# Kernel optimization log

Hardware: AMD Instinct MI355X
Metric: run time of the kernel (lower is better)

## Reference

```python
import jax, jax.numpy as jnp
import numpy as np

NHEADS = 8
KSIZE = 15
DILATION = 1


def _local_mask(N, ksize, d):
    # eye(N) + sum_i eye(N, k=+/-(d*i)) for i in 1..ksize//2  -> banded boolean mask
    K = ksize // 2
    m = np.eye(N)
    for i in range(1, K + 1):
        m += np.eye(N, k=d * i) + np.eye(N, k=-d * i)
    return jnp.asarray(m > 0)


def _nl(x, mask, cW, cb, vW, vb, lm):
    """NonLocalBlock: keys from v_lin, queries/values from c_lin split; per-head
    scores mk @ mq^T / sqrt(dh), banded local mask + segment mask, softmax over
    last axis, residual add. drop_prob=0 so dropout is identity."""
    B, L, D = x.shape
    odim = vW.shape[1]
    dh = odim // NHEADS
    neg = jnp.asarray(-1e9, x.dtype)
    mk = (x @ vW + vb).reshape(B, L, NHEADS, dh)
    ct = x @ cW + cb                      # [B,L,2*odim]
    mq = ct[..., :odim].reshape(B, L, NHEADS, dh)
    mv = ct[..., odim:].reshape(B, L, NHEADS, dh)
    s = jnp.einsum('blhd,bmhd->bhlm', mk, mq) / jnp.sqrt(jnp.asarray(dh, x.dtype))
    if lm is not None:
        s = jnp.where(lm[None, None], s, neg)
    s = jnp.where((mask != 0)[:, None, None, :], s, neg)
    w = jax.nn.softmax(s, axis=-1)
    r = jnp.einsum('bhlm,bmhd->blhd', w, mv).reshape(B, L, odim)
    return x + r


def setup_inputs() -> dict:
    key = jax.random.key(0)
    ks = jax.random.split(key, 24)
    B, L, D, N = 16, 512, 512, 3
    NL_LOCAL, NL_GLOBAL, AH = 2, 2, 256
    sc = 0.02
    rn = lambda k, shp: jax.random.normal(k, shp, jnp.float32) * sc
    return {
        'seg_feats': jax.random.normal(ks[0], (B, L, D), jnp.float32),
        'seg_masks': jnp.ones((B, L), jnp.float32),
        'se_feats': jax.random.normal(ks[1], (B, N, D), jnp.float32),
        # HadamardProduct params, one per semantic entity (stacked on axis 0)
        'hp_w1': rn(ks[2], (N, D, D)), 'hp_b1': jnp.zeros((N, D), jnp.float32),
        'hp_w2': rn(ks[3], (N, D, D)), 'hp_b2': jnp.zeros((N, D), jnp.float32),
        'hp_w3': rn(ks[4], (N, D, D)), 'hp_b3': jnp.zeros((N, D), jnp.float32),
        # local masked non-local blocks: [N, n_local_mnl, ...]
        'local_cW': rn(ks[5], (N, NL_LOCAL, D, 2 * D)),
        'local_cb': jnp.zeros((N, NL_LOCAL, 2 * D), jnp.float32),
        'local_vW': rn(ks[6], (N, NL_LOCAL, D, D)),
        'local_vb': jnp.zeros((N, NL_LOCAL, D), jnp.float32),
        # global non-local blocks: [n_global_nl, ...]
        'global_cW': rn(ks[7], (NL_GLOBAL, D, 2 * D)),
        'global_cb': jnp.zeros((NL_GLOBAL, 2 * D), jnp.float32),
        'global_vW': rn(ks[8], (NL_GLOBAL, D, D)),
        'global_vb': jnp.zeros((NL_GLOBAL, D), jnp.float32),
        # AttentivePooling over semantic entities (no bias, no embedding fc)
        'satt_w1': rn(ks[9], (D, AH)),
        'satt_w2': rn(ks[10], (AH, 1)),
    }


def reference(seg_feats, seg_masks, se_feats,
              hp_w1, hp_b1, hp_w2, hp_b2, hp_w3, hp_b3,
              local_cW, local_cb, local_vW, local_vb,
              global_cW, global_cb, global_vW, global_vb,
              satt_w1, satt_w2):
    B, L, D = seg_feats.shape
    N = se_feats.shape[1]
    # 1) segment-level modality fusion (HadamardProduct per semantic entity)
    h1 = jax.nn.relu(jnp.einsum('bld,ndh->bnlh', seg_feats, hp_w1) + hp_b1[None, :, None, :])
    h2 = jax.nn.relu(jnp.einsum('bnd,ndh->bnh', se_feats, hp_w2) + hp_b2[None])
    m = jax.nn.relu(jnp.einsum('bnlh,nhk->bnlk', h1 * h2[:, :, None, :], hp_w3)
                    + hp_b3[None, :, None, :])  # [B,N,L,D]
    # 2) local context modeling: masked non-local blocks with banded mask
    lm = _local_mask(L, KSIZE, DILATION)
    ss = []
    for n in range(N):
        f = m[:, n]
        for s in range(local_cW.shape[1]):
            f = _nl(f, seg_masks, local_cW[n, s], local_cb[n, s],
                    local_vW[n, s], local_vb[n, s], lm)
        ss.append(f)
    ss = jnp.stack(ss, axis=1)  # [B,N,L,D]
    # 3) semantic attentive pooling over entities -> weighted sum of ss_feats
    alpha = jnp.tanh(se_feats @ satt_w1) @ satt_w2       # [B,N,1]
    sattw = jax.nn.softmax(alpha[..., 0], axis=1)        # [B,N]
    a = jnp.einsum('bn,bnld->bld', sattw, ss)            # [B,L,D]
    # 4) global context modeling: plain non-local blocks (no local mask)
    for s in range(global_cW.shape[0]):
        a = _nl(a, seg_masks, global_cW[s], global_cb[s], global_vW[s], global_vb[s], None)
    return a, sattw
```

## Files before the change

### kernel.cpp

```cpp
#include <hip/hip_runtime.h>
#include <hip/hip_bf16.h>

#define BB 16
#define LL 512
#define DD 512
#define NSEG 3
#define NH 8
#define DH 64
#define AH 256

typedef __attribute__((ext_vector_type(4))) float f32x4;
typedef __attribute__((ext_vector_type(8))) short s16x8;

__device__ __forceinline__ unsigned short f2b(float f) {
  union { float f; unsigned u; } c; c.f = f;
  unsigned r = (c.u + 0x7FFF + ((c.u >> 16) & 1)) >> 16;
  return (unsigned short)r;
}

#define PADK 40
__global__ __launch_bounds__(256) void mfma_gemm(
    const float* __restrict__ A, const float* __restrict__ W,
    const float* __restrict__ bias, float* __restrict__ C,
    int Nc, int K, long bsA, long bsC, int act)
{
  __shared__ unsigned short As[64 * PADK];
  __shared__ unsigned short Bs[64 * PADK];
  const int tid = threadIdx.x;
  const int lane = tid & 63, wv = tid >> 6;
  const float* Ab = A + (long)blockIdx.z * bsA + (long)blockIdx.y * 64 * K;
  const float* Wb = W + blockIdx.x * 64;
  float* Cb = C + (long)blockIdx.z * bsC + (long)blockIdx.y * 64 * Nc + blockIdx.x * 64;

  const int arow = tid >> 2, akq = tid & 3;
  const int bkp = tid & 15, bnq = tid >> 4;
  const int fr = lane & 15, fk = (lane >> 4) * 8;

  f32x4 acc[4] = {};
  for (int k0 = 0; k0 < K; k0 += 32) {
    {
      const float* ap = Ab + (long)arow * K + k0 + akq * 8;
      float4 a0 = *(const float4*)ap;
      float4 a1 = *(const float4*)(ap + 4);
      union { unsigned short h[8]; uint4 v; } u;
      u.h[0] = f2b(a0.x); u.h[1] = f2b(a0.y); u.h[2] = f2b(a0.z); u.h[3] = f2b(a0.w);
      u.h[4] = f2b(a1.x); u.h[5] = f2b(a1.y); u.h[6] = f2b(a1.z); u.h[7] = f2b(a1.w);
      *(uint4*)&As[arow * PADK + akq * 8] = u.v;
    }
    {
      const float* wp = Wb + (long)(k0 + 2 * bkp) * Nc + 4 * bnq;
      float4 w0 = *(const float4*)wp;
      float4 w1 = *(const float4*)(wp + Nc);
      unsigned* bsw = (unsigned*)Bs;
      bsw[(4 * bnq + 0) * (PADK / 2) + bkp] = (unsigned)f2b(w0.x) | ((unsigned)f2b(w1.x) << 16);
      bsw[(4 * bnq + 1) * (PADK / 2) + bkp] = (unsigned)f2b(w0.y) | ((unsigned)f2b(w1.y) << 16);
      bsw[(4 * bnq + 2) * (PADK / 2) + bkp] = (unsigned)f2b(w0.z) | ((unsigned)f2b(w1.z) << 16);
      bsw[(4 * bnq + 3) * (PADK / 2) + bkp] = (unsigned)f2b(w0.w) | ((unsigned)f2b(w1.w) << 16);
    }
    __syncthreads();
    s16x8 af = *(const s16x8*)&As[(wv * 16 + fr) * PADK + fk];
#pragma unroll
    for (int nt = 0; nt < 4; ++nt) {
      s16x8 bf = *(const s16x8*)&Bs[(nt * 16 + fr) * PADK + fk];
      acc[nt] = __builtin_amdgcn_mfma_f32_16x16x32_bf16(af, bf, acc[nt], 0, 0, 0);
    }
    __syncthreads();
  }
  const int rowb = wv * 16 + (lane >> 4) * 4;
  const int colb = lane & 15;
#pragma unroll
  for (int nt = 0; nt < 4; ++nt) {
    const float bv = bias[blockIdx.x * 64 + nt * 16 + colb];
#pragma unroll
    for (int j = 0; j < 4; ++j) {
      float v = acc[nt][j] + bv;
      if (act) v = fmaxf(v, 0.f);
      Cb[(long)(rowb + j) * Nc + nt * 16 + colb] = v;
    }
  }
}

__global__ __launch_bounds__(256) void h2_kernel(
    const float* __restrict__ se, const float* __restrict__ w2,
    const float* __restrict__ b2, float* __restrict__ h2)
{
  __shared__ float ses[DD];
  const int bn = blockIdx.x;
  const int n = bn % NSEG;
  const int t = threadIdx.x;
  ses[t] = se[(long)bn * DD + t];
  ses[t + 256] = se[(long)bn * DD + t + 256];
  __syncthreads();
  const float* wn = w2 + (long)n * DD * DD;
  for (int j = t; j < DD; j += 256) {
    float acc = b2[n * DD + j];
    for (int k = 0; k < DD; ++k) acc = fmaf(ses[k], wn[(long)k * DD + j], acc);
    h2[(long)bn * DD + j] = fmaxf(acc, 0.f);
  }
}

__global__ __launch_bounds__(256) void mult_kernel(float* __restrict__ h1,
                                                   const float* __restrict__ h2)
{
  long i4 = (long)blockIdx.x * 256 + threadIdx.x;
  float4 v = ((float4*)h1)[i4];
  long bn = i4 >> 16;
  int d4 = (int)(i4 & 127);
  float4 m = ((const float4*)h2)[bn * 128 + d4];
  v.x *= m.x; v.y *= m.y; v.z *= m.z; v.w *= m.w;
  ((float4*)h1)[i4] = v;
}

__global__ __launch_bounds__(512) void local_attn(
    float* __restrict__ x, const float* __restrict__ mk,
    const float* __restrict__ ct, const float* __restrict__ mask, long bsX)
{
  const int l = blockIdx.x, b = blockIdx.y;
  const int t = threadIdx.x;
  const int h = t >> 6, d = t & 63;
  const float mkv = mk[((long)b * LL + l) * DD + h * DH + d];
  const float* ctb = ct + (long)b * LL * (2 * DD);
  const float* mb = mask + (long)b * LL;
  float sc[15];
#pragma unroll
  for (int i = 0; i < 15; ++i) {
    int m = l - 7 + i;
    bool valid = (m >= 0) && (m < LL);
    int mc = valid ? m : 0;
    float p = mkv * ctb[(long)mc * (2 * DD) + h * DH + d];
#pragma unroll
    for (int o = 32; o > 0; o >>= 1) p += __shfl_xor(p, o, 64);
    float s = p * 0.125f;
    if (mb[mc] == 0.f) s = -1e9f;
    sc[i] = valid ? s : -3e9f;
  }
  float mx = sc[0];
#pragma unroll
  for (int i = 1; i < 15; ++i) mx = fmaxf(mx, sc[i]);
  float sum = 0.f;
#pragma unroll
  for (int i = 0; i < 15; ++i) { sc[i] = __expf(sc[i] - mx); sum += sc[i]; }
  const float inv = 1.f / sum;
  float r = 0.f;
#pragma unroll
  for (int i = 0; i < 15; ++i) {
    int m = l - 7 + i;
    int mc = (m < 0) ? 0 : ((m >= LL) ? (LL - 1) : m);
    r = fmaf(sc[i], ctb[(long)mc * (2 * DD) + DD + h * DH + d], r);
  }
  x[(long)b * bsX + (long)l * DD + h * DH + d] += r * inv;
}

__global__ __launch_bounds__(256) void score_kernel(
    const float* __restrict__ mk, const float* __restrict__ ct,
    const float* __restrict__ msk, float* __restrict__ S, int b0)
{
  __shared__ float As[64][65];
  __shared__ float Bs[64][65];
  const int bz = blockIdx.z;
  const int bl = bz >> 3, h = bz & 7;
  const int t = threadIdx.x;
  const float* Ab = mk + ((long)bl * LL + blockIdx.y * 64) * DD + h * DH;
  const float* Bb = ct + ((long)bl * LL + blockIdx.x * 64) * (2 * DD) + h * DH;
  {
    int r = t >> 2, c0 = (t & 3) << 4;
#pragma unroll
    for (int i = 0; i < 4; ++i) {
      int c = c0 + i * 4;
      float4 a = *(const float4*)(Ab + (long)r * DD + c);
      As[c][r] = a.x; As[c + 1][r] = a.y; As[c + 2][r] = a.z; As[c + 3][r] = a.w;
      float4 q = *(const float4*)(Bb + (long)r * (2 * DD) + c);
      Bs[c][r] = q.x; Bs[c + 1][r] = q.y; Bs[c + 2][r] = q.z; Bs[c + 3][r] = q.w;
    }
  }
  __syncthreads();
  const int tx = t & 15, ty = t >> 4;
  float acc[4][4] = {};
#pragma unroll 8
  for (int d = 0; d < 64; ++d) {
    float a4[4], b4[4];
#pragma unroll
    for (int i = 0; i < 4; ++i) { a4[i] = As[d][(ty << 2) + i]; b4[i] = Bs[d][(tx << 2) + i]; }
#pragma unroll
    for (int i = 0; i < 4; ++i)
#pragma unroll
      for (int j = 0; j < 4; ++j) acc[i][j] = fmaf(a4[i], b4[j], acc[i][j]);
  }
  const float* mrow = msk + (long)(b0 + bl) * LL + blockIdx.x * 64 + (tx << 2);
  float mv[4];
#pragma unroll
  for (int j = 0; j < 4; ++j) mv[j] = mrow[j];
  float* Sb = S + ((long)bz * LL + blockIdx.y * 64) * LL + blockIdx.x * 64;
#pragma unroll
  for (int i = 0; i < 4; ++i) {
    float4 o;
    float* op = &o.x;
#pragma unroll
    for (int j = 0; j < 4; ++j)
      op[j] = (mv[j] == 0.f) ? -1e9f : acc[i][j] * 0.125f;
    *(float4*)(Sb + (long)((ty << 2) + i) * LL + (tx << 2)) = o;
  }
}

__global__ __launch_bounds__(256) void smax_kernel(float* __restrict__ S)
{
  const int w = threadIdx.x >> 6, lane = threadIdx.x & 63;
  long row = (long)blockIdx.x * 4 + w;
  float* p = S + row * LL;
  float v[8];
  float mx = -3e38f;
#pragma unroll
  for (int i = 0; i < 8; ++i) { v[i] = p[lane + i * 64]; mx = fmaxf(mx, v[i]); }
#pragma unroll
  for (int o = 32; o > 0; o >>= 1) mx = fmaxf(mx, __shfl_xor(mx, o, 64));
  float sum = 0.f;
#pragma unroll
  for (int i = 0; i < 8; ++i) { v[i] = __expf(v[i] - mx); sum += v[i]; }
#pragma unroll
  for (int o = 32; o > 0; o >>= 1) sum += __shfl_xor(sum, o, 64);
  const float inv = 1.f / sum;
#pragma unroll
  for (int i = 0; i < 8; ++i) p[lane + i * 64] = v[i] * inv;
}

__global__ __launch_bounds__(256) void pv_kernel(
    const float* __restrict__ S, const float* __restrict__ ct,
    float* __restrict__ out, int b0)
{
  __shared__ float As[32][68];
  __shared__ float Bs[32][68];
  const int bz = blockIdx.y;
  const int bl = bz >> 3, h = bz & 7;
  const float* Ab = S + ((long)bz * LL + blockIdx.x * 64) * LL;
  const float* Bb = ct + (long)bl * LL * (2 * DD) + DD + h * DH;
  float* Cb = out + ((long)(b0 + bl) * LL + blockIdx.x * 64) * DD + h * DH;
  const int tid = threadIdx.x;
  const int tx = tid & 15, ty = tid >> 4;
  float acc[4][4] = {};
  for (int k0 = 0; k0 < LL; k0 += 32) {
#pragma unroll
    for (int i = 0; i < 2; ++i) {
      int idx = tid + i * 256;
      int r = idx >> 3, kc = (idx & 7) << 2;
      float4 av = *(const float4*)(Ab + (long)r * LL + k0 + kc);
      As[kc][r] = av.x; As[kc + 1][r] = av.y; As[kc + 2][r] = av.z; As[kc + 3][r] = av.w;
      int kk = idx >> 4, nc = (idx & 15) << 2;
      float4 bv = *(const float4*)(Bb + (long)(k0 + kk) * (2 * DD) + nc);
      *(float4*)&Bs[kk][nc] = bv;
    }
    __syncthreads();
#pragma unroll
    for (int kk = 0; kk < 32; ++kk) {
      float4 a4 = *(const float4*)&As[kk][ty << 2];
      float4 b4 = *(const float4*)&Bs[kk][tx << 2];
      float av[4] = {a4.x, a4.y, a4.z, a4.w};
      float bv[4] = {b4.x, b4.y, b4.z, b4.w};
#pragma unroll
      for (int i = 0; i < 4; ++i)
#pragma unroll
        for (int j = 0; j < 4; ++j) acc[i][j] = fmaf(av[i], bv[j], acc[i][j]);
    }
    __syncthreads();
  }
#pragma unroll
  for (int i = 0; i < 4; ++i) {
    float* cp = Cb + (long)((ty << 2) + i) * DD + (tx << 2);
    float4 o = *(const float4*)cp;
    o.x += acc[i][0]; o.y += acc[i][1]; o.z += acc[i][2]; o.w += acc[i][3];
    *(float4*)cp = o;
  }
}

__global__ __launch_bounds__(256) void alpha_kernel(
    const float* __restrict__ se, const float* __restrict__ w1,
    const float* __restrict__ w2, float* __restrict__ alpha)
{
  __shared__ float ses[DD];
  __shared__ float red[4];
  const int bn = blockIdx.x;
  const int t = threadIdx.x;
  ses[t] = se[(long)bn * DD + t];
  ses[t + 256] = se[(long)bn * DD + t + 256];
  __syncthreads();
  float acc = 0.f;
  for (int k = 0; k < DD; ++k) acc = fmaf(ses[k], w1[(long)k * AH + t], acc);
  float v = tanhf(acc) * w2[t];
#pragma unroll
  for (int o = 32; o > 0; o >>= 1) v += __shfl_xor(v, o, 64);
  if ((t & 63) == 0) red[t >> 6] = v;
  __syncthreads();
  if (t == 0) alpha[bn] = red[0] + red[1] + red[2] + red[3];
}

__global__ __launch_bounds__(128) void mix_kernel(
    const float* __restrict__ xbuf, const float* __restrict__ alpha,
    float* __restrict__ abuf, float* __restrict__ outw)
{
  const int l = blockIdx.x, b = blockIdx.y;
  const float a0 = alpha[b * 3 + 0], a1 = alpha[b * 3 + 1], a2 = alpha[b * 3 + 2];
  const float mx = fmaxf(a0, fmaxf(a1, a2));
  const float e0 = __expf(a0 - mx), e1 = __expf(a1 - mx), e2 = __expf(a2 - mx);
  const float inv = 1.f / (e0 + e1 + e2);
  const float w0 = e0 * inv, w1 = e1 * inv, w2 = e2 * inv;
  const float4* x0 = (const float4*)(xbuf + (((long)b * 3 + 0) * LL + l) * DD);
  const float4* x1 = (const float4*)(xbuf + (((long)b * 3 + 1) * LL + l) * DD);
  const float4* x2 = (const float4*)(xbuf + (((long)b * 3 + 2) * LL + l) * DD);
  float4* ar = (float4*)(abuf + ((long)b * LL + l) * DD);
  const int t = threadIdx.x;
  float4 v0 = x0[t], v1 = x1[t], v2 = x2[t];
  float4 o;
  o.x = w0 * v0.x + w1 * v1.x + w2 * v2.x;
  o.y = w0 * v0.y + w1 * v1.y + w2 * v2.y;
  o.z = w0 * v0.z + w1 * v1.z + w2 * v2.z;
  o.w = w0 * v0.w + w1 * v1.w + w2 * v2.w;
  ar[t] = o;
  if (l == 0 && t < 3) {
    float wv = (t == 0) ? w0 : ((t == 1) ? w1 : w2);
    outw[b * 3 + t] = wv;
  }
}

extern "C" void kernel_launch(void* const* d_in, const int* in_sizes, int n_in,
                              void* d_out, int out_size, void* d_ws, size_t ws_size,
                              hipStream_t stream) {
  const float* seg = (const float*)d_in[0];
  const float* msk = (const float*)d_in[1];
  const float* se  = (const float*)d_in[2];
  const float* w1  = (const float*)d_in[3];
  const float* b1  = (const float*)d_in[4];
  const float* w2  = (const float*)d_in[5];
  const float* b2  = (const float*)d_in[6];
  const float* w3  = (const float*)d_in[7];
  const float* b3  = (const float*)d_in[8];
  const float* lcW = (const float*)d_in[9];
  const float* lcb = (const float*)d_in[10];
  const float* lvW = (const float*)d_in[11];
  const float* lvb = (const float*)d_in[12];
  const float* gcW = (const float*)d_in[13];
  const float* gcb = (const float*)d_in[14];
  const float* gvW = (const float*)d_in[15];
  const float* gvb = (const float*)d_in[16];
  const float* sw1 = (const float*)d_in[17];
  const float* sw2 = (const float*)d_in[18];
  float* out = (float*)d_out;

  const long LD = (long)LL * DD;
  const long DDDD = (long)DD * DD;
  float* ws = (float*)d_ws;
  float* xbuf = ws;
  float* scratch = xbuf + (long)BB * NSEG * LD;
  float* mkbuf = scratch;
  float* ctbuf = scratch + (long)BB * LD;
  float* h2buf = scratch + (long)BB * NSEG * LD;
  float* alphabuf = h2buf + (long)BB * NSEG * DD;
  float* Sbuf = ws;
  float* mkc  = ws + 16777216;
  float* ctc  = mkc + 2097152;

  dim3 g88(8, 8, BB), g168(16, 8, BB), blk(256);

  h2_kernel<<<BB * NSEG, 256, 0, stream>>>(se, w2, b2, h2buf);
  for (int n = 0; n < NSEG; ++n)
    mfma_gemm<<<g88, blk, 0, stream>>>(seg, w1 + (long)n * DDDD, b1 + n * DD,
                                       scratch + n * LD, DD, DD, LD, NSEG * LD, 1);
  mult_kernel<<<12288, 256, 0, stream>>>(scratch, h2buf);
  for (int n = 0; n < NSEG; ++n)
    mfma_gemm<<<g88, blk, 0, stream>>>(scratch + n * LD, w3 + (long)n * DDDD, b3 + n * DD,
                                       xbuf + n * LD, DD, DD, NSEG * LD, NSEG * LD, 1);

  for (int n = 0; n < NSEG; ++n)
    for (int s = 0; s < 2; ++s) {
      const float* vWp = lvW + (long)(n * 2 + s) * DDDD;
      const float* vbp = lvb + (long)(n * 2 + s) * DD;
      const float* cWp = lcW + (long)(n * 2 + s) * 2 * DDDD;
      const float* cbp = lcb + (long)(n * 2 + s) * 2 * DD;
      mfma_gemm<<<g88, blk, 0, stream>>>(xbuf + n * LD, vWp, vbp, mkbuf,
                                         DD, DD, NSEG * LD, LD, 0);
      mfma_gemm<<<g168, blk, 0, stream>>>(xbuf + n * LD, cWp, cbp, ctbuf,
                                          2 * DD, DD, NSEG * LD, 2 * LD, 0);
      local_attn<<<dim3(LL, BB), 512, 0, stream>>>(xbuf + n * LD, mkbuf, ctbuf, msk,
                                                   (long)NSEG * LD);
    }

  alpha_kernel<<<BB * NSEG, 256, 0, stream>>>(se, sw1, sw2, alphabuf);
  mix_kernel<<<dim3(LL, BB), 128, 0, stream>>>(xbuf, alphabuf, out, out + 4194304);

  const int CHB = 8;
  for (int c = 0; c < BB / CHB; ++c) {
    const int b0 = c * CHB;
    float* outc = out + (long)b0 * LD;
    for (int s = 0; s < 2; ++s) {
      mfma_gemm<<<dim3(8, 8, CHB), blk, 0, stream>>>(
          outc, gvW + (long)s * DDDD, gvb + (long)s * DD, mkc, DD, DD, LD, LD, 0);
      mfma_gemm<<<dim3(16, 8, CHB), blk, 0, stream>>>(
          outc, gcW + (long)s * 2 * DDDD, gcb + (long)s * 2 * DD, ctc,
          2 * DD, DD, LD, 2 * LD, 0);
      score_kernel<<<dim3(8, 8, CHB * NH), blk, 0, stream>>>(mkc, ctc, msk, Sbuf, b0);
      smax_kernel<<<CHB * NH * LL / 4, 256, 0, stream>>>(Sbuf);
      pv_kernel<<<dim3(8, CHB * NH), blk, 0, stream>>>(Sbuf, ctc, out, b0);
    }
  }
}
```

Measured before the change: 1.766 ms.

## Pre-cast GEMM operands to bf16 and vectorize local attention scoring

Adds cast kernels that convert activations and weights to bf16 once, so the MFMA GEMM loads bf16 tiles directly. Before, each block converted fp32 to bf16 on every tile, repeated across all column blocks. The Hadamard multiply is fused into a cast kernel. The global blocks now cast each layer's input once instead of once per chunk. local_attn now computes the 15 banded scores in parallel, with 4 lanes per neighbour doing float4 dot products, replacing 15 full-wave shuffle reductions. The cost is extra launches and bf16 staging buffers in the workspace.

```diff
diff --git a/kernel.cpp b/kernel.cpp
--- a/kernel.cpp
+++ b/kernel.cpp
@@ -11,6 +11,7 @@
 
 typedef __attribute__((ext_vector_type(4))) float f32x4;
 typedef __attribute__((ext_vector_type(8))) short s16x8;
+typedef unsigned short ushort_t;
 
 __device__ __forceinline__ unsigned short f2b(float f) {
   union { float f; unsigned u; } c; c.f = f;
@@ -18,18 +19,56 @@
   return (unsigned short)r;
 }
 
+__global__ __launch_bounds__(256) void castb(
+    const float* __restrict__ src, long bstride, int shift,
+    ushort_t* __restrict__ dst)
+{
+  long idx8 = (long)blockIdx.x * 256 + threadIdx.x;
+  long b = idx8 >> shift;
+  long r8 = idx8 & ((1L << shift) - 1);
+  const float* p = src + b * bstride + r8 * 8;
+  float4 a = *(const float4*)p;
+  float4 c = *(const float4*)(p + 4);
+  union { ushort_t h[8]; uint4 v; } u;
+  u.h[0] = f2b(a.x); u.h[1] = f2b(a.y); u.h[2] = f2b(a.z); u.h[3] = f2b(a.w);
+  u.h[4] = f2b(c.x); u.h[5] = f2b(c.y); u.h[6] = f2b(c.z); u.h[7] = f2b(c.w);
+  *(uint4*)(dst + idx8 * 8) = u.v;
+}
+
+__global__ __launch_bounds__(256) void mult_cast(
+    const float* __restrict__ h1, const float* __restrict__ h2, int n,
+    ushort_t* __restrict__ dst)
+{
+  long idx8 = (long)blockIdx.x * 256 + threadIdx.x;
+  long b = idx8 >> 15;
+  long r8 = idx8 & 32767;
+  int d0 = (int)(r8 & 63) * 8;
+  const float* p = h1 + b * (3 * (long)LL * DD) + r8 * 8;
+  const float* q = h2 + (b * 3 + n) * DD + d0;
+  float4 a = *(const float4*)p;
+  float4 c = *(const float4*)(p + 4);
+  float4 m0 = *(const float4*)q;
+  float4 m1 = *(const float4*)(q + 4);
+  union { ushort_t h[8]; uint4 v; } u;
+  u.h[0] = f2b(a.x * m0.x); u.h[1] = f2b(a.y * m0.y);
+  u.h[2] = f2b(a.z * m0.z); u.h[3] = f2b(a.w * m0.w);
+  u.h[4] = f2b(c.x * m1.x); u.h[5] = f2b(c.y * m1.y);
+  u.h[6] = f2b(c.z * m1.z); u.h[7] = f2b(c.w * m1.w);
+  *(uint4*)(dst + idx8 * 8) = u.v;
+}
+
 #define PADK 40
 __global__ __launch_bounds__(256) void mfma_gemm(
-    const float* __restrict__ A, const float* __restrict__ W,
+    const ushort_t* __restrict__ A, const ushort_t* __restrict__ W,
     const float* __restrict__ bias, float* __restrict__ C,
     int Nc, int K, long bsA, long bsC, int act)
 {
-  __shared__ unsigned short As[64 * PADK];
-  __shared__ unsigned short Bs[64 * PADK];
+  __shared__ ushort_t As[64 * PADK];
+  __shared__ ushort_t Bs[64 * PADK];
   const int tid = threadIdx.x;
   const int lane = tid & 63, wv = tid >> 6;
-  const float* Ab = A + (long)blockIdx.z * bsA + (long)blockIdx.y * 64 * K;
-  const float* Wb = W + blockIdx.x * 64;
+  const ushort_t* Ab = A + (long)blockIdx.z * bsA + (long)blockIdx.y * 64 * K;
+  const ushort_t* Wb = W + blockIdx.x * 64;
   float* Cb = C + (long)blockIdx.z * bsC + (long)blockIdx.y * 64 * Nc + blockIdx.x * 64;
 
   const int arow = tid >> 2, akq = tid & 3;
@@ -38,24 +77,17 @@
 
   f32x4 acc[4] = {};
   for (int k0 = 0; k0 < K; k0 += 32) {
+    *(uint4*)&As[arow * PADK + akq * 8] =
+        *(const uint4*)(Ab + (long)arow * K + k0 + akq * 8);
     {
-      const float* ap = Ab + (long)arow * K + k0 + akq * 8;
-      float4 a0 = *(const float4*)ap;
-      float4 a1 = *(const float4*)(ap + 4);
-      union { unsigned short h[8]; uint4 v; } u;
-      u.h[0] = f2b(a0.x); u.h[1] = f2b(a0.y); u.h[2] = f2b(a0.z); u.h[3] = f2b(a0.w);
-      u.h[4] = f2b(a1.x); u.h[5] = f2b(a1.y); u.h[6] = f2b(a1.z); u.h[7] = f2b(a1.w);
-      *(uint4*)&As[arow * PADK + akq * 8] = u.v;
-    }
-    {
-      const float* wp = Wb + (long)(k0 + 2 * bkp) * Nc + 4 * bnq;
-      float4 w0 = *(const float4*)wp;
-      float4 w1 = *(const float4*)(wp + Nc);
+      const ushort_t* wp = Wb + (long)(k0 + 2 * bkp) * Nc + 4 * bnq;
+      ushort4 w0 = *(const ushort4*)wp;
+      ushort4 w1 = *(const ushort4*)(wp + Nc);
       unsigned* bsw = (unsigned*)Bs;
-      bsw[(4 * bnq + 0) * (PADK / 2) + bkp] = (unsigned)f2b(w0.x) | ((unsigned)f2b(w1.x) << 16);
-      bsw[(4 * bnq + 1) * (PADK / 2) + bkp] = (unsigned)f2b(w0.y) | ((unsigned)f2b(w1.y) << 16);
-      bsw[(4 * bnq + 2) * (PADK / 2) + bkp] = (unsigned)f2b(w0.z) | ((unsigned)f2b(w1.z) << 16);
-      bsw[(4 * bnq + 3) * (PADK / 2) + bkp] = (unsigned)f2b(w0.w) | ((unsigned)f2b(w1.w) << 16);
+      bsw[(4 * bnq + 0) * (PADK / 2) + bkp] = (unsigned)w0.x | ((unsigned)w1.x << 16);
+      bsw[(4 * bnq + 1) * (PADK / 2) + bkp] = (unsigned)w0.y | ((unsigned)w1.y << 16);
+      bsw[(4 * bnq + 2) * (PADK / 2) + bkp] = (unsigned)w0.z | ((unsigned)w1.z << 16);
+      bsw[(4 * bnq + 3) * (PADK / 2) + bkp] = (unsigned)w0.w | ((unsigned)w1.w << 16);
     }
     __syncthreads();
     s16x8 af = *(const s16x8*)&As[(wv * 16 + fr) * PADK + fk];
@@ -99,41 +131,36 @@
   }
 }
 
-__global__ __launch_bounds__(256) void mult_kernel(float* __restrict__ h1,
-                                                   const float* __restrict__ h2)
-{
-  long i4 = (long)blockIdx.x * 256 + threadIdx.x;
-  float4 v = ((float4*)h1)[i4];
-  long bn = i4 >> 16;
-  int d4 = (int)(i4 & 127);
-  float4 m = ((const float4*)h2)[bn * 128 + d4];
-  v.x *= m.x; v.y *= m.y; v.z *= m.z; v.w *= m.w;
-  ((float4*)h1)[i4] = v;
-}
-
 __global__ __launch_bounds__(512) void local_attn(
     float* __restrict__ x, const float* __restrict__ mk,
     const float* __restrict__ ct, const float* __restrict__ mask, long bsX)
 {
   const int l = blockIdx.x, b = blockIdx.y;
   const int t = threadIdx.x;
-  const int h = t >> 6, d = t & 63;
-  const float mkv = mk[((long)b * LL + l) * DD + h * DH + d];
+  const int h = t >> 6, lane = t & 63;
+  const int grp = lane >> 2, r4 = lane & 3;
   const float* ctb = ct + (long)b * LL * (2 * DD);
   const float* mb = mask + (long)b * LL;
+  int m = l - 7 + grp;
+  bool valid = (grp < 15) && (m >= 0) && (m < LL);
+  int mc = valid ? m : 0;
+  const float* mkp = mk + ((long)b * LL + l) * DD + h * DH + r4 * 16;
+  const float* mqp = ctb + (long)mc * (2 * DD) + h * DH + r4 * 16;
+  float dot = 0.f;
+#pragma unroll
+  for (int j = 0; j < 16; j += 4) {
+    float4 a = *(const float4*)(mkp + j);
+    float4 q = *(const float4*)(mqp + j);
+    dot = fmaf(a.x, q.x, fmaf(a.y, q.y, fmaf(a.z, q.z, fmaf(a.w, q.w, dot))));
+  }
+  dot += __shfl_xor(dot, 1, 64);
+  dot += __shfl_xor(dot, 2, 64);
+  float s = dot * 0.125f;
+  if (mb[mc] == 0.f) s = -1e9f;
+  if (!valid) s = -3e9f;
   float sc[15];
 #pragma unroll
-  for (int i = 0; i < 15; ++i) {
-    int m = l - 7 + i;
-    bool valid = (m >= 0) && (m < LL);
-    int mc = valid ? m : 0;
-    float p = mkv * ctb[(long)mc * (2 * DD) + h * DH + d];
-#pragma unroll
-    for (int o = 32; o > 0; o >>= 1) p += __shfl_xor(p, o, 64);
-    float s = p * 0.125f;
-    if (mb[mc] == 0.f) s = -1e9f;
-    sc[i] = valid ? s : -3e9f;
-  }
+  for (int i = 0; i < 15; ++i) sc[i] = __shfl(s, i * 4, 64);
   float mx = sc[0];
 #pragma unroll
   for (int i = 1; i < 15; ++i) mx = fmaxf(mx, sc[i]);
@@ -144,11 +171,11 @@
   float r = 0.f;
 #pragma unroll
   for (int i = 0; i < 15; ++i) {
-    int m = l - 7 + i;
-    int mc = (m < 0) ? 0 : ((m >= LL) ? (LL - 1) : m);
-    r = fmaf(sc[i], ctb[(long)mc * (2 * DD) + DD + h * DH + d], r);
-  }
-  x[(long)b * bsX + (long)l * DD + h * DH + d] += r * inv;
+    int mm = l - 7 + i;
+    int mcc = (mm < 0) ? 0 : ((mm >= LL) ? (LL - 1) : mm);
+    r = fmaf(sc[i], ctb[(long)mcc * (2 * DD) + DD + h * DH + lane], r);
+  }
+  x[(long)b * bsX + (long)l * DD + h * DH + lane] += r * inv;
 }
 
 __global__ __launch_bounds__(256) void score_kernel(
@@ -353,6 +380,9 @@
   float* ctbuf = scratch + (long)BB * LD;
   float* h2buf = scratch + (long)BB * NSEG * LD;
   float* alphabuf = h2buf + (long)BB * NSEG * DD;
+  ushort_t* xb16 = (ushort_t*)(alphabuf + 64);
+  ushort_t* wbA = xb16 + (long)BB * LD;
+  ushort_t* wbB = wbA + 2 * DDDD;
   float* Sbuf = ws;
   float* mkc  = ws + 16777216;
   float* ctc  = mkc + 2097152;
@@ -360,24 +390,29 @@
   dim3 g88(8, 8, BB), g168(16, 8, BB), blk(256);
 
   h2_kernel<<<BB * NSEG, 256, 0, stream>>>(se, w2, b2, h2buf);
-  for (int n = 0; n < NSEG; ++n)
-    mfma_gemm<<<g88, blk, 0, stream>>>(seg, w1 + (long)n * DDDD, b1 + n * DD,
+  castb<<<2048, 256, 0, stream>>>(seg, 0, 22, xb16);
+  for (int n = 0; n < NSEG; ++n) {
+    castb<<<128, 256, 0, stream>>>(w1 + (long)n * DDDD, 0, 22, wbB);
+    mfma_gemm<<<g88, blk, 0, stream>>>(xb16, wbB, b1 + n * DD,
                                        scratch + n * LD, DD, DD, LD, NSEG * LD, 1);
-  mult_kernel<<<12288, 256, 0, stream>>>(scratch, h2buf);
-  for (int n = 0; n < NSEG; ++n)
-    mfma_gemm<<<g88, blk, 0, stream>>>(scratch + n * LD, w3 + (long)n * DDDD, b3 + n * DD,
-                                       xbuf + n * LD, DD, DD, NSEG * LD, NSEG * LD, 1);
+  }
+  for (int n = 0; n < NSEG; ++n) {
+    mult_cast<<<2048, 256, 0, stream>>>(scratch + n * LD, h2buf, n, xb16);
+    castb<<<128, 256, 0, stream>>>(w3 + (long)n * DDDD, 0, 22, wbB);
+    mfma_gemm<<<g88, blk, 0, stream>>>(xb16, wbB, b3 + n * DD,
+                                       xbuf + n * LD, DD, DD, LD, NSEG * LD, 1);
+  }
 
   for (int n = 0; n < NSEG; ++n)
     for (int s = 0; s < 2; ++s) {
-      const float* vWp = lvW + (long)(n * 2 + s) * DDDD;
-      const float* vbp = lvb + (long)(n * 2 + s) * DD;
-      const float* cWp = lcW + (long)(n * 2 + s) * 2 * DDDD;
-      const float* cbp = lcb + (long)(n * 2 + s) * 2 * DD;
-      mfma_gemm<<<g88, blk, 0, stream>>>(xbuf + n * LD, vWp, vbp, mkbuf,
-                                         DD, DD, NSEG * LD, LD, 0);
-      mfma_gemm<<<g168, blk, 0, stream>>>(xbuf + n * LD, cWp, cbp, ctbuf,
-                                          2 * DD, DD, NSEG * LD, 2 * LD, 0);
+      const int i = n * 2 + s;
+      castb<<<2048, 256, 0, stream>>>(xbuf + n * LD, NSEG * LD, 15, xb16);
+      castb<<<128, 256, 0, stream>>>(lvW + (long)i * DDDD, 0, 22, wbB);
+      castb<<<256, 256, 0, stream>>>(lcW + (long)i * 2 * DDDD, 0, 22, wbA);
+      mfma_gemm<<<g88, blk, 0, stream>>>(xb16, wbB, lvb + (long)i * DD,
+                                         mkbuf, DD, DD, LD, LD, 0);
+      mfma_gemm<<<g168, blk, 0, stream>>>(xb16, wbA, lcb + (long)i * 2 * DD,
+                                          ctbuf, 2 * DD, DD, LD, 2 * LD, 0);
       local_attn<<<dim3(LL, BB), 512, 0, stream>>>(xbuf + n * LD, mkbuf, ctbuf, msk,
                                                    (long)NSEG * LD);
     }
@@ -386,14 +421,16 @@
   mix_kernel<<<dim3(LL, BB), 128, 0, stream>>>(xbuf, alphabuf, out, out + 4194304);
 
   const int CHB = 8;
-  for (int c = 0; c < BB / CHB; ++c) {
-    const int b0 = c * CHB;
-    float* outc = out + (long)b0 * LD;
-    for (int s = 0; s < 2; ++s) {
+  for (int s = 0; s < 2; ++s) {
+    castb<<<2048, 256, 0, stream>>>(out, 0, 22, xb16);
+    castb<<<128, 256, 0, stream>>>(gvW + (long)s * DDDD, 0, 22, wbB);
+    castb<<<256, 256, 0, stream>>>(gcW + (long)s * 2 * DDDD, 0, 22, wbA);
+    for (int c = 0; c < BB / CHB; ++c) {
+      const int b0 = c * CHB;
       mfma_gemm<<<dim3(8, 8, CHB), blk, 0, stream>>>(
-          outc, gvW + (long)s * DDDD, gvb + (long)s * DD, mkc, DD, DD, LD, LD, 0);
+          xb16 + (long)b0 * LD, wbB, gvb + (long)s * DD, mkc, DD, DD, LD, LD, 0);
       mfma_gemm<<<dim3(16, 8, CHB), blk, 0, stream>>>(
-          outc, gcW + (long)s * 2 * DDDD, gcb + (long)s * 2 * DD, ctc,
+          xb16 + (long)b0 * LD, wbA, gcb + (long)s * 2 * DD, ctc,
           2 * DD, DD, LD, 2 * LD, 0);
       score_kernel<<<dim3(8, 8, CHB * NH), blk, 0, stream>>>(mkc, ctc, msk, Sbuf, b0);
       smax_kernel<<<CHB * NH * LL / 4, 256, 0, stream>>>(Sbuf);
```

After: 1.594 ms. 1.11x faster.
